# Optimization experiments

Hardware: AMD Instinct MI355X
Metric: run time of the kernel (lower is better)

The kernel has to match this reference:

```python
import jax, jax.numpy as jnp
import numpy as np

N_NODES = 100000
N_EDGES = 800000
D_IN = 256
D_HID = 256
D_OUT = 64
HEADS = 1
ALPHA = 0.5          # TransConv residual weight
GRAPH_WEIGHT = 0.8   # _SGFormer aggregate='add' weight
LN_EPS = 1e-5
BN_EPS = 1e-5


def layer_norm(x, g, b):
    mu = x.mean(-1, keepdims=True)
    var = ((x - mu) ** 2).mean(-1, keepdims=True)
    return (x - mu) * jax.lax.rsqrt(var + LN_EPS) * g + b


def full_attention_conv(qs, ks, vs):
    # qs, ks, vs: [N, H, C]; normalization is by the GLOBAL Frobenius norm
    qs = qs / jnp.linalg.norm(qs)
    ks = ks / jnp.linalg.norm(ks)
    N = qs.shape[0]
    kvs = jnp.einsum('lhm,lhd->hmd', ks, vs)                     # [H,C,C]
    attention_num = jnp.einsum('nhm,hmd->nhd', qs, kvs) + N * vs  # [N,H,C]
    ks_sum = ks.sum(axis=0)                                      # [H,C]
    normalizer = jnp.einsum('nhm,hm->nh', qs, ks_sum)[..., None] + N
    return attention_num / normalizer


def gcn_conv(x, src, dst, w, b, n):
    # PyG GCNConv: h = x @ W; add self-loops; D^-1/2 (A+I) D^-1/2 h; + bias
    h = x @ w
    loop = jnp.arange(n)
    s = jnp.concatenate([src, loop])
    d = jnp.concatenate([dst, loop])
    deg = jax.ops.segment_sum(jnp.ones_like(s, dtype=h.dtype), d, num_segments=n)
    dinv = jnp.where(deg > 0, jax.lax.rsqrt(jnp.maximum(deg, 1e-12)), 0.0)
    norm = dinv[s] * dinv[d]
    out = jax.ops.segment_sum(h[s] * norm[:, None], d, num_segments=n)
    return out + b


def setup_inputs() -> dict:
    key = jax.random.key(0)
    ks = jax.random.split(key, 24)
    f32 = jnp.float32
    def lin(k, fi, fo):
        s = 1.0 / np.sqrt(fi)
        kw, kb = jax.random.split(k)
        return (jax.random.uniform(kw, (fi, fo), f32, -s, s),
                jax.random.uniform(kb, (fo,), f32, -s, s))
    x = jax.random.normal(ks[0], (N_NODES, D_IN), f32)
    edge_index = jax.random.randint(ks[1], (2, N_EDGES), 0, N_NODES, jnp.int64)
    fc0_w, fc0_b = lin(ks[2], D_IN, D_HID)
    wq0_w, wq0_b = lin(ks[3], D_HID, D_HID * HEADS)
    wk0_w, wk0_b = lin(ks[4], D_HID, D_HID * HEADS)
    wv0_w, wv0_b = lin(ks[5], D_HID, D_HID * HEADS)
    wq1_w, wq1_b = lin(ks[6], D_HID, D_HID * HEADS)
    wk1_w, wk1_b = lin(ks[7], D_HID, D_HID * HEADS)
    wv1_w, wv1_b = lin(ks[8], D_HID, D_HID * HEADS)
    gcn_w0, gcn_b0 = lin(ks[9], D_IN, D_HID)
    gcn_w1, gcn_b1 = lin(ks[10], D_HID, D_HID)
    fc_w, fc_b = lin(ks[11], D_HID, D_OUT)
    ones = jnp.ones((D_HID,), f32)
    zeros = jnp.zeros((D_HID,), f32)
    return dict(
        x=x, edge_index=edge_index,
        fc0_w=fc0_w, fc0_b=fc0_b, ln0_g=ones, ln0_b=zeros,
        wq0_w=wq0_w, wq0_b=wq0_b, wk0_w=wk0_w, wk0_b=wk0_b, wv0_w=wv0_w, wv0_b=wv0_b,
        ln1_g=ones, ln1_b=zeros,
        wq1_w=wq1_w, wq1_b=wq1_b, wk1_w=wk1_w, wk1_b=wk1_b, wv1_w=wv1_w, wv1_b=wv1_b,
        ln2_g=ones, ln2_b=zeros,
        gcn_w0=gcn_w0, gcn_b0=gcn_b0, bn_g=ones, bn_b=zeros,
        gcn_w1=gcn_w1, gcn_b1=gcn_b1,
        fc_w=fc_w, fc_b=fc_b)


def reference(x, edge_index, fc0_w, fc0_b, ln0_g, ln0_b,
              wq0_w, wq0_b, wk0_w, wk0_b, wv0_w, wv0_b, ln1_g, ln1_b,
              wq1_w, wq1_b, wk1_w, wk1_b, wv1_w, wv1_b, ln2_g, ln2_b,
              gcn_w0, gcn_b0, bn_g, bn_b, gcn_w1, gcn_b1, fc_w, fc_b):
    n = x.shape[0]
    src, dst = edge_index[0], edge_index[1]
    # ---- TransConv (eval mode: dropout = identity) ----
    h = layer_norm(x @ fc0_w + fc0_b, ln0_g, ln0_b)
    h = jax.nn.relu(h)
    layer_params = [
        (wq0_w, wq0_b, wk0_w, wk0_b, wv0_w, wv0_b, ln1_g, ln1_b),
        (wq1_w, wq1_b, wk1_w, wk1_b, wv1_w, wv1_b, ln2_g, ln2_b),
    ]
    for (qw, qb, kw, kb, vw, vb, lg, lb) in layer_params:
        q = (h @ qw + qb).reshape(n, HEADS, D_HID)
        k = (h @ kw + kb).reshape(n, HEADS, D_HID)
        v = (h @ vw + vb).reshape(n, HEADS, D_HID)
        a = full_attention_conv(q, k, v).mean(axis=1)   # mean over heads
        h = layer_norm(ALPHA * a + (1.0 - ALPHA) * h, lg, lb)
    x_trans = h
    # ---- GCN branch (BN in eval: running_mean=0, running_var=1) ----
    g = gcn_conv(x, src, dst, gcn_w0, gcn_b0, n)
    g = g * (bn_g / jnp.sqrt(1.0 + BN_EPS)) + bn_b
    g = jax.nn.relu(g)
    g = gcn_conv(g, src, dst, gcn_w1, gcn_b1, n)
    # ---- combine + classifier ----
    emb = GRAPH_WEIGHT * g + (1.0 - GRAPH_WEIGHT) * x_trans
    return emb @ fc_w + fc_b
```

## Files before the change

### kernel.cpp

```cpp
#include <hip/hip_runtime.h>
#include <hip/hip_bf16.h>

#define NN 100000
#define NE 800000
#define DH 256
#define DOUT 64
#define NSPL 50000
#define NSO ((size_t)NSPL * DH)
#define NBLK 391

using bf16 = __hip_bfloat16;
typedef __attribute__((ext_vector_type(8))) short bf16x8;
typedef __attribute__((ext_vector_type(4))) float f32x4;

__device__ __forceinline__ float bits2f(unsigned short h) {
    union { unsigned int u; float f; } c; c.u = ((unsigned int)h) << 16; return c.f;
}
__device__ __forceinline__ unsigned short f2b(float v) {
    union { float f; unsigned int u; } c; c.f = v;
    unsigned int u = c.u;
    return (unsigned short)((u + 0x7FFFu + ((u >> 16) & 1u)) >> 16);
}
__device__ __forceinline__ unsigned short tob(float v) { return f2b(v); }
__device__ __forceinline__ unsigned short tob(bf16 v) {
    union { bf16 b; unsigned short u; } c; c.b = v; return c.u;
}
__device__ __forceinline__ float ldf(const void* p, size_t i, int isbf) {
    if (isbf) return bits2f(((const unsigned short*)p)[i]);
    return ((const float*)p)[i];
}
__device__ __forceinline__ float ldS(const float* p, size_t i) { return p[i]; }
__device__ __forceinline__ float ldS(const bf16* p, size_t i) { return __bfloat162float(p[i]); }
__device__ __forceinline__ void stS(float* p, size_t i, float v) { p[i] = v; }
__device__ __forceinline__ void stS(bf16* p, size_t i, float v) { p[i] = __float2bfloat16(v); }
__device__ __forceinline__ float4 ld4S(const float* p) { return *(const float4*)p; }
__device__ __forceinline__ float4 ld4S(const bf16* p) {
    ushort4 u = *(const ushort4*)(const void*)p;
    return make_float4(bits2f(u.x), bits2f(u.y), bits2f(u.z), bits2f(u.w));
}
__device__ __forceinline__ void st4S(float* p, float4 v) { *(float4*)p = v; }
__device__ __forceinline__ void st4S(bf16* p, float4 v) {
    *(ushort4*)(void*)p = make_ushort4(f2b(v.x), f2b(v.y), f2b(v.z), f2b(v.w));
}
__device__ __forceinline__ void ld8(const void* p, size_t idx, int isbf, ushort4& o0, ushort4& o1) {
    if (isbf) {
        const ushort4* q = (const ushort4*)((const unsigned short*)p + idx);
        o0 = q[0]; o1 = q[1];
    } else {
        const float4* q = (const float4*)((const float*)p + idx);
        float4 a = q[0], b = q[1];
        o0 = make_ushort4(f2b(a.x), f2b(a.y), f2b(a.z), f2b(a.w));
        o1 = make_ushort4(f2b(b.x), f2b(b.y), f2b(b.z), f2b(b.w));
    }
}
__device__ __forceinline__ void ld8S(const bf16* p, size_t idx, ushort4& o0, ushort4& o1) {
    const ushort4* q = (const ushort4*)((const unsigned short*)p + idx);
    o0 = q[0]; o1 = q[1];
}
__device__ __forceinline__ void ld8S(const float* p, size_t idx, ushort4& o0, ushort4& o1) {
    const float4* q = (const float4*)(p + idx);
    float4 a = q[0], b = q[1];
    o0 = make_ushort4(f2b(a.x), f2b(a.y), f2b(a.z), f2b(a.w));
    o1 = make_ushort4(f2b(b.x), f2b(b.y), f2b(b.z), f2b(b.w));
}
__device__ __forceinline__ int ld_src(const int* ei, int e, int i64) {
    return i64 ? ei[2 * (size_t)e] : ei[e];
}
__device__ __forceinline__ int ld_dst(const int* ei, int e, int i64) {
    return i64 ? ei[2 * ((size_t)NE + e)] : ei[NE + e];
}

__global__ __launch_bounds__(256) void detect_kernel(const void* x, const int* ei, int* flags)
{
    __shared__ int s_sane[4], s_nz[4];
    int t = threadIdx.x;
    const unsigned short* xu = (const unsigned short*)x;
    int sane = 0;
    for (int i = t; i < 2048; i += 256) {
        float v = bits2f(xu[2 * i]);
        float a = fabsf(v);
        if (v == v && a > 1e-3f && a < 100.f) sane++;
    }
    int nz = 0;
    for (int i = t; i < 4096; i += 256) {
        if (ei[2 * (i * 122) + 1] != 0) nz++;
    }
#pragma unroll
    for (int off = 32; off > 0; off >>= 1) { sane += __shfl_down(sane, off); nz += __shfl_down(nz, off); }
    if ((t & 63) == 0) { s_sane[t >> 6] = sane; s_nz[t >> 6] = nz; }
    __syncthreads();
    if (t == 0) {
        flags[0] = ((s_sane[0] + s_sane[1] + s_sane[2] + s_sane[3]) > 1024) ? 1 : 0;
        flags[1] = ((s_nz[0] + s_nz[1] + s_nz[2] + s_nz[3]) == 0) ? 1 : 0;
    }
}

template <typename ST>
__global__ __launch_bounds__(512) void gemm_mfma(
    const void* __restrict__ A, const void* __restrict__ W,
    const void* __restrict__ bias, ST* __restrict__ C,
    int M, int Nc, const int* __restrict__ flags, int a_sel)
{
    __shared__ unsigned short Bs[64][264];
    const int isbf = flags[0];
    const int abf = (a_sel == 2) ? isbf : a_sel;
    const int tid = threadIdx.x;
    const int wave = tid >> 6, lane = tid & 63;
    const int quad = lane >> 4, nl = lane & 15;
    const int m0 = blockIdx.x * 128;
    const int n0 = blockIdx.y * 64;

    const int arow = m0 + wave * 16 + nl;
    const int av = (arow < M);
    const size_t abase = (size_t)arow * DH + quad * 8;
    ushort4 pa0[8], pa1[8];
#pragma unroll
    for (int s = 0; s < 8; ++s) {
        if (av) ld8(A, abase + s * 32, abf, pa0[s], pa1[s]);
        else { pa0[s] = make_ushort4(0, 0, 0, 0); pa1[s] = pa0[s]; }
    }

#pragma unroll
    for (int it = 0; it < 4; ++it) {
        int p8 = it * 512 + tid;
        int k = p8 >> 3, nb = p8 & 7;
        ushort4 w0, w1;
        ld8(W, (size_t)k * Nc + n0 + nb * 8, isbf, w0, w1);
        int nbase = nb * 8;
        Bs[nbase + 0][k] = w0.x; Bs[nbase + 1][k] = w0.y;
        Bs[nbase + 2][k] = w0.z; Bs[nbase + 3][k] = w0.w;
        Bs[nbase + 4][k] = w1.x; Bs[nbase + 5][k] = w1.y;
        Bs[nbase + 6][k] = w1.z; Bs[nbase + 7][k] = w1.w;
    }
    __syncthreads();

    f32x4 acc[4] = {{0.f,0.f,0.f,0.f},{0.f,0.f,0.f,0.f},{0.f,0.f,0.f,0.f},{0.f,0.f,0.f,0.f}};

#pragma unroll
    for (int s = 0; s < 8; ++s) {
        const int k0 = s * 32;
        bf16x8 af;
        ((ushort4*)&af)[0] = pa0[s]; ((ushort4*)&af)[1] = pa1[s];
#pragma unroll
        for (int ct = 0; ct < 4; ++ct) {
            bf16x8 bfg = *(const bf16x8*)&Bs[ct * 16 + nl][k0 + quad * 8];
            acc[ct] = __builtin_amdgcn_mfma_f32_16x16x32_bf16(af, bfg, acc[ct], 0, 0, 0);
        }
    }

#pragma unroll
    for (int ct = 0; ct < 4; ++ct) {
        int n = n0 + ct * 16 + nl;
        float bv = bias ? ldf(bias, n, isbf) : 0.f;
#pragma unroll
        for (int r = 0; r < 4; ++r) {
            int m = m0 + wave * 16 + quad * 4 + r;
            if (m < M) stS(C, (size_t)m * Nc + n, acc[ct][r] + bv);
        }
    }
}

template <typename ST>
__global__ __launch_bounds__(256) void kvs_mfma(
    const ST* __restrict__ Am, const ST* __restrict__ Bm, float* __restrict__ D)
{
    __shared__ unsigned short Ast[64][36];
    __shared__ unsigned short Bst[64][36];
    const int tid = threadIdx.x;
    const int wave = tid >> 6, lane = tid & 63;
    const int quad = lane >> 4, nl = lane & 15;
    const int i0 = blockIdx.x * 64, j0 = blockIdx.y * 64;
    const int S = gridDim.z;
    const int chunk = (NN + S - 1) / S;
    const int ns = blockIdx.z * chunk;
    const int ne = min(ns + chunk, NN);
    const int nn = tid >> 3;
    const int c0 = (tid & 7) * 8;
    f32x4 acc[4] = {{0.f,0.f,0.f,0.f},{0.f,0.f,0.f,0.f},{0.f,0.f,0.f,0.f},{0.f,0.f,0.f,0.f}};

    for (int n0 = ns; n0 < ne; n0 += 32) {
        int n = n0 + nn;
        ushort4 a0, a1, b0, b1;
        if (n < ne) {
            ld8S(Am, (size_t)n * DH + i0 + c0, a0, a1);
            ld8S(Bm, (size_t)n * DH + j0 + c0, b0, b1);
        } else {
            a0 = make_ushort4(0, 0, 0, 0); a1 = a0; b0 = a0; b1 = a0;
        }
        __syncthreads();
        Ast[c0 + 0][nn] = a0.x; Ast[c0 + 1][nn] = a0.y;
        Ast[c0 + 2][nn] = a0.z; Ast[c0 + 3][nn] = a0.w;
        Ast[c0 + 4][nn] = a1.x; Ast[c0 + 5][nn] = a1.y;
        Ast[c0 + 6][nn] = a1.z; Ast[c0 + 7][nn] = a1.w;
        Bst[c0 + 0][nn] = b0.x; Bst[c0 + 1][nn] = b0.y;
        Bst[c0 + 2][nn] = b0.z; Bst[c0 + 3][nn] = b0.w;
        Bst[c0 + 4][nn] = b1.x; Bst[c0 + 5][nn] = b1.y;
        Bst[c0 + 6][nn] = b1.z; Bst[c0 + 7][nn] = b1.w;
        __syncthreads();
        bf16x8 af = *(const bf16x8*)&Ast[wave * 16 + nl][quad * 8];
#pragma unroll
        for (int ct = 0; ct < 4; ++ct) {
            bf16x8 bfg = *(const bf16x8*)&Bst[ct * 16 + nl][quad * 8];
            acc[ct] = __builtin_amdgcn_mfma_f32_16x16x32_bf16(af, bfg, acc[ct], 0, 0, 0);
        }
    }
#pragma unroll
    for (int ct = 0; ct < 4; ++ct)
#pragma unroll
        for (int r = 0; r < 4; ++r)
            atomicAdd(&D[(size_t)(i0 + wave * 16 + quad * 4 + r) * DH + j0 + ct * 16 + nl], acc[ct][r]);
}

__global__ __launch_bounds__(256) void kvs2b_kernel(const float* __restrict__ kvs,
                                                    unsigned short* __restrict__ kvsb)
{
    int i = blockIdx.x * 256 + threadIdx.x;
    size_t o = (size_t)i * 8;
    float4 a = *(const float4*)(kvs + o);
    float4 b = *(const float4*)(kvs + o + 4);
    *(ushort4*)(kvsb + o)     = make_ushort4(f2b(a.x), f2b(a.y), f2b(a.z), f2b(a.w));
    *(ushort4*)(kvsb + o + 4) = make_ushort4(f2b(b.x), f2b(b.y), f2b(b.z), f2b(b.w));
}

template <typename ST>
__global__ __launch_bounds__(256) void attn_mfma(
    const ST* __restrict__ Q, const ST* __restrict__ V,
    const unsigned short* __restrict__ kvsb, const float* __restrict__ ks_sum,
    const float* __restrict__ qss, const float* __restrict__ kss,
    ST* __restrict__ out)
{
    __shared__ float ks_s[DH];
    __shared__ float nrm_s[64];
    const int tid = threadIdx.x;
    const int wave = tid >> 6, lane = tid & 63;
    const int quad = lane >> 4, nl = lane & 15;
    const int m0 = blockIdx.x * 64;
    const int j0 = blockIdx.y * 128;

    const int arow = m0 + wave * 16 + nl;
    const int av = (arow < NN);
    const size_t abase = (size_t)arow * DH + quad * 8;
    ushort4 pq0[8], pq1[8];
#pragma unroll
    for (int s = 0; s < 8; ++s) {
        if (av) ld8S(Q, abase + s * 32, pq0[s], pq1[s]);
        else { pq0[s] = make_ushort4(0, 0, 0, 0); pq1[s] = pq0[s]; }
    }

    ks_s[tid] = ks_sum[tid];
    __syncthreads();

    f32x4 acc[8];
#pragma unroll
    for (int i = 0; i < 8; ++i) acc[i] = (f32x4){0.f, 0.f, 0.f, 0.f};
    float nrm = 0.f;

#pragma unroll
    for (int s = 0; s < 8; ++s) {
        const int k0 = s * 32;
        bf16x8 af;
        ((ushort4*)&af)[0] = pq0[s]; ((ushort4*)&af)[1] = pq1[s];
#pragma unroll
        for (int j = 0; j < 8; ++j)
            nrm += bits2f(((const unsigned short*)&af)[j]) * ks_s[k0 + quad * 8 + j];
        const unsigned short* kb = kvsb + (size_t)(j0 + nl) * DH + k0 + quad * 8;
#pragma unroll
        for (int ct = 0; ct < 8; ++ct) {
            bf16x8 bfg = *(const bf16x8*)(kb + (size_t)ct * 16 * DH);
            acc[ct] = __builtin_amdgcn_mfma_f32_16x16x32_bf16(af, bfg, acc[ct], 0, 0, 0);
        }
    }
    nrm += __shfl_xor(nrm, 16);
    nrm += __shfl_xor(nrm, 32);
    if (lane < 16) nrm_s[wave * 16 + lane] = nrm;
    __syncthreads();
    const float scale = rsqrtf(*qss) * rsqrtf(*kss);
#pragma unroll
    for (int r = 0; r < 4; ++r) {
        int row = m0 + wave * 16 + quad * 4 + r;
        if (row >= NN) continue;
        float den = nrm_s[wave * 16 + quad * 4 + r] * scale + (float)NN;
#pragma unroll
        for (int ct = 0; ct < 8; ++ct) {
            int col = j0 + ct * 16 + nl;
            float v = ldS(V, (size_t)row * DH + col);
            float numv = acc[ct][r] * scale + (float)NN * v;
            stS(out, (size_t)row * DH + col, numv / den);
        }
    }
}

template <typename ST>
__global__ __launch_bounds__(256) void ln_kernel(
    const ST* __restrict__ A, const ST* __restrict__ B,
    float alpha, float beta,
    const void* __restrict__ g, const void* __restrict__ b,
    ST* __restrict__ out, int relu, const int* __restrict__ flags)
{
    const int isbf = flags[0];
    const int wave = threadIdx.x >> 6, lane = threadIdx.x & 63;
    const int row = blockIdx.x * 4 + wave;
    if (row >= NN) return;
    const size_t base = (size_t)row * DH + lane * 4;
    float4 v = ld4S(&A[base]);
    v.x *= alpha; v.y *= alpha; v.z *= alpha; v.w *= alpha;
    if (B) {
        float4 w = ld4S(&B[base]);
        v.x += beta * w.x; v.y += beta * w.y; v.z += beta * w.z; v.w += beta * w.w;
    }
    float s = v.x + v.y + v.z + v.w;
    float s2 = v.x * v.x + v.y * v.y + v.z * v.z + v.w * v.w;
#pragma unroll
    for (int off = 32; off > 0; off >>= 1) {
        s += __shfl_xor(s, off);
        s2 += __shfl_xor(s2, off);
    }
    float mean = s * (1.f / DH);
    float var = s2 * (1.f / DH) - mean * mean;
    float rstd = rsqrtf(var + 1e-5f);
    float4 o;
    o.x = (v.x - mean) * rstd * ldf(g, lane * 4 + 0, isbf) + ldf(b, lane * 4 + 0, isbf);
    o.y = (v.y - mean) * rstd * ldf(g, lane * 4 + 1, isbf) + ldf(b, lane * 4 + 1, isbf);
    o.z = (v.z - mean) * rstd * ldf(g, lane * 4 + 2, isbf) + ldf(b, lane * 4 + 2, isbf);
    o.w = (v.w - mean) * rstd * ldf(g, lane * 4 + 3, isbf) + ldf(b, lane * 4 + 3, isbf);
    if (relu) {
        o.x = fmaxf(o.x, 0.f); o.y = fmaxf(o.y, 0.f);
        o.z = fmaxf(o.z, 0.f); o.w = fmaxf(o.w, 0.f);
    }
    st4S(&out[base], o);
}

template <typename ST>
__global__ __launch_bounds__(256) void sumsq_kernel(
    const ST* __restrict__ A, size_t n, float* __restrict__ out)
{
    __shared__ float ps[4];
    size_t i = (size_t)blockIdx.x * blockDim.x + threadIdx.x;
    size_t stride = (size_t)gridDim.x * blockDim.x;
    float s = 0.f;
    for (; i < n; i += stride) { float v = ldS(A, i); s += v * v; }
#pragma unroll
    for (int off = 32; off > 0; off >>= 1) s += __shfl_down(s, off);
    if ((threadIdx.x & 63) == 0) ps[threadIdx.x >> 6] = s;
    __syncthreads();
    if (threadIdx.x == 0) atomicAdd(out, ps[0] + ps[1] + ps[2] + ps[3]);
}

template <typename ST>
__global__ __launch_bounds__(256) void colsum_kernel(
    const ST* __restrict__ Km, float* __restrict__ out)
{
    const int t = threadIdx.x;
    const int per = (NN + gridDim.x - 1) / gridDim.x;
    size_t r0 = (size_t)blockIdx.x * per;
    size_t r1 = r0 + per; if (r1 > NN) r1 = NN;
    float s = 0.f;
    for (size_t r = r0; r < r1; ++r) s += ldS(Km, r * DH + t);
    atomicAdd(&out[t], s);
}

__global__ __launch_bounds__(256) void count_kernel(const int* __restrict__ ei, int* __restrict__ cnt,
                                                    const int* __restrict__ flags)
{
    int e = blockIdx.x * 256 + threadIdx.x;
    if (e >= NE) return;
    int d = ld_dst(ei, e, flags[1]);
    if ((unsigned)d < NN) atomicAdd(&cnt[d], 1);
}

__global__ __launch_bounds__(256) void scan_block_kernel(const int* __restrict__ cnt,
                                                         int* __restrict__ pre, int* __restrict__ bsum)
{
    __shared__ int s[256];
    int i = blockIdx.x * 256 + threadIdx.x;
    int v = (i < NN) ? cnt[i] : 0;
    s[threadIdx.x] = v;
    __syncthreads();
    for (int off = 1; off < 256; off <<= 1) {
        int t = (threadIdx.x >= off) ? s[threadIdx.x - off] : 0;
        __syncthreads();
        s[threadIdx.x] += t;
        __syncthreads();
    }
    if (i < NN) pre[i] = s[threadIdx.x] - v;
    if (threadIdx.x == 255) bsum[blockIdx.x] = s[255];
}

__global__ __launch_bounds__(512) void scan_partial_kernel(int* __restrict__ bsum, int nb)
{
    __shared__ int s[512];
    int t = threadIdx.x;
    int v = (t < nb) ? bsum[t] : 0;
    s[t] = v;
    __syncthreads();
    for (int off = 1; off < 512; off <<= 1) {
        int u = (t >= off) ? s[t - off] : 0;
        __syncthreads();
        s[t] += u;
        __syncthreads();
    }
    if (t < nb) bsum[t] = s[t] - v;
}

__global__ __launch_bounds__(256) void finalize_kernel(int* __restrict__ base, const int* __restrict__ bsum,
                                                       const int* __restrict__ cnt, int* __restrict__ cursor,
                                                       float* __restrict__ dinv)
{
    int i = blockIdx.x * 256 + threadIdx.x;
    if (i >= NN) return;
    int b = base[i] + bsum[blockIdx.x];
    base[i] = b;
    cursor[i] = b;
    dinv[i] = rsqrtf((float)cnt[i] + 1.0f);
}

__global__ __launch_bounds__(256) void scatter_kernel(const int* __restrict__ ei, int* __restrict__ cursor,
                                                      int* __restrict__ srcs, const int* __restrict__ flags)
{
    int e = blockIdx.x * 256 + threadIdx.x;
    if (e >= NE) return;
    int i64 = flags[1];
    int s = ld_src(ei, e, i64), d = ld_dst(ei, e, i64);
    if ((unsigned)s >= NN || (unsigned)d >= NN) return;
    int pos = atomicAdd(&cursor[d], 1);
    srcs[pos] = s;
}

template <typename ST, int MODE>
__global__ __launch_bounds__(256) void fgather_kernel(
    const ST* __restrict__ Hs, const ST* __restrict__ Ht,
    const int* __restrict__ base, const int* __restrict__ cnt,
    const int* __restrict__ srcs, const float* __restrict__ dinv,
    const void* __restrict__ bias, const void* __restrict__ bng, const void* __restrict__ bnb,
    const int* __restrict__ flags, ST* __restrict__ out)
{
    const int isbf = flags[0];
    int node = blockIdx.x * 4 + (threadIdx.x >> 6);
    int lane = threadIdx.x & 63;
    if (node >= NN) return;
    int b0 = base[node], deg = cnt[node];
    float dd = dinv[node];
    float4 a0 = make_float4(0.f, 0.f, 0.f, 0.f);
    float4 a1 = make_float4(0.f, 0.f, 0.f, 0.f);
    int j = 0;
    for (; j + 4 <= deg; j += 4) {
        int s0 = srcs[b0 + j + 0], s1 = srcs[b0 + j + 1];
        int s2 = srcs[b0 + j + 2], s3 = srcs[b0 + j + 3];
        float n0 = dd * dinv[s0], n1 = dd * dinv[s1];
        float n2 = dd * dinv[s2], n3 = dd * dinv[s3];
        float4 h0 = ld4S(&Hs[(size_t)s0 * DH + lane * 4]);
        float4 h1 = ld4S(&Hs[(size_t)s1 * DH + lane * 4]);
        float4 h2 = ld4S(&Hs[(size_t)s2 * DH + lane * 4]);
        float4 h3 = ld4S(&Hs[(size_t)s3 * DH + lane * 4]);
        a0.x += h0.x * n0; a0.y += h0.y * n0; a0.z += h0.z * n0; a0.w += h0.w * n0;
        a1.x += h1.x * n1; a1.y += h1.y * n1; a1.z += h1.z * n1; a1.w += h1.w * n1;
        a0.x += h2.x * n2; a0.y += h2.y * n2; a0.z += h2.z * n2; a0.w += h2.w * n2;
        a1.x += h3.x * n3; a1.y += h3.y * n3; a1.z += h3.z * n3; a1.w += h3.w * n3;
    }
    for (; j < deg; ++j) {
        int s0 = srcs[b0 + j];
        float n0 = dd * dinv[s0];
        float4 h0 = ld4S(&Hs[(size_t)s0 * DH + lane * 4]);
        a0.x += h0.x * n0; a0.y += h0.y * n0; a0.z += h0.z * n0; a0.w += h0.w * n0;
    }
    const size_t obase = (size_t)node * DH + lane * 4;
    float4 own = ld4S(&Hs[obase]);
    float di2 = dd * dd;
    int c = lane * 4;
    float4 v;
    v.x = a0.x + a1.x + own.x * di2 + ldf(bias, c + 0, isbf);
    v.y = a0.y + a1.y + own.y * di2 + ldf(bias, c + 1, isbf);
    v.z = a0.z + a1.z + own.z * di2 + ldf(bias, c + 2, isbf);
    v.w = a0.w + a1.w + own.w * di2 + ldf(bias, c + 3, isbf);
    if (MODE == 0) {
        const float bnscale = 0.99999500003749981f;
        v.x = fmaxf(v.x * (ldf(bng, c + 0, isbf) * bnscale) + ldf(bnb, c + 0, isbf), 0.f);
        v.y = fmaxf(v.y * (ldf(bng, c + 1, isbf) * bnscale) + ldf(bnb, c + 1, isbf), 0.f);
        v.z = fmaxf(v.z * (ldf(bng, c + 2, isbf) * bnscale) + ldf(bnb, c + 2, isbf), 0.f);
        v.w = fmaxf(v.w * (ldf(bng, c + 3, isbf) * bnscale) + ldf(bnb, c + 3, isbf), 0.f);
    } else {
        float4 t = ld4S(&Ht[obase]);
        v.x = 0.8f * v.x + 0.2f * t.x;
        v.y = 0.8f * v.y + 0.2f * t.y;
        v.z = 0.8f * v.z + 0.2f * t.z;
        v.w = 0.8f * v.w + 0.2f * t.w;
    }
    st4S(&out[obase], v);
}

__global__ __launch_bounds__(256) void deg_kernel(const int* __restrict__ ei, float* __restrict__ deg,
                                                  const int* __restrict__ flags)
{
    int i64 = flags[1];
    int e = blockIdx.x * 256 + threadIdx.x;
    if (e >= NE) return;
    int d = ld_dst(ei, e, i64);
    if ((unsigned)d < NN) atomicAdd(&deg[d], 1.0f);
}

__global__ __launch_bounds__(256) void dinv_kernel(float* __restrict__ deg)
{
    int i = blockIdx.x * 256 + threadIdx.x;
    if (i < NN) deg[i] = rsqrtf(deg[i] + 1.0f);
}

template <typename ST>
__global__ __launch_bounds__(256) void agg_kernel(
    const ST* __restrict__ Hs, const int* __restrict__ ei,
    const float* __restrict__ dinv, float* __restrict__ lo, float* __restrict__ hi,
    const int* __restrict__ flags)
{
    int i64 = flags[1];
    int e = blockIdx.x * 4 + (threadIdx.x >> 6);
    int lane = threadIdx.x & 63;
    if (e >= NE) return;
    int s = ld_src(ei, e, i64), d = ld_dst(ei, e, i64);
    if ((unsigned)s >= NN || (unsigned)d >= NN) return;
    float nrm = dinv[s] * dinv[d];
    const float4 h4 = ld4S(&Hs[(size_t)s * DH + lane * 4]);
    float* o = (d < NSPL ? &lo[(size_t)d * DH] : &hi[(size_t)(d - NSPL) * DH]) + lane * 4;
    atomicAdd(o + 0, h4.x * nrm);
    atomicAdd(o + 1, h4.y * nrm);
    atomicAdd(o + 2, h4.z * nrm);
    atomicAdd(o + 3, h4.w * nrm);
}

template <typename ST>
__global__ __launch_bounds__(256) void gcn_epi1_kernel(
    const float* __restrict__ lo, const float* __restrict__ hi,
    const ST* __restrict__ h1, const float* __restrict__ dinv,
    const void* __restrict__ b0, const void* __restrict__ bng, const void* __restrict__ bnb,
    const int* __restrict__ flags, ST* __restrict__ out)
{
    const int isbf = flags[0];
    size_t idx = (size_t)blockIdx.x * 256 + threadIdx.x;
    if (idx >= (size_t)NN * DH) return;
    int i = (int)(idx >> 8), c = (int)(idx & 255);
    float aggv = (i < NSPL) ? lo[idx] : hi[idx - NSO];
    float di = dinv[i];
    float v = aggv + ldS(h1, idx) * di * di + ldf(b0, c, isbf);
    const float bnscale = 0.99999500003749981f;
    v = v * (ldf(bng, c, isbf) * bnscale) + ldf(bnb, c, isbf);
    stS(out, idx, fmaxf(v, 0.f));
}

template <typename ST>
__global__ __launch_bounds__(256) void gcn_epi2_kernel(
    const float* __restrict__ lo, const float* __restrict__ hi,
    const ST* __restrict__ h2, const ST* __restrict__ Ht, const float* __restrict__ dinv,
    const void* __restrict__ b1, const int* __restrict__ flags, ST* __restrict__ out)
{
    const int isbf = flags[0];
    size_t idx = (size_t)blockIdx.x * 256 + threadIdx.x;
    if (idx >= (size_t)NN * DH) return;
    int i = (int)(idx >> 8), c = (int)(idx & 255);
    float aggv = (i < NSPL) ? lo[idx] : hi[idx - NSO];
    float di = dinv[i];
    float g = aggv + ldS(h2, idx) * di * di + ldf(b1, c, isbf);
    stS(out, idx, 0.8f * g + 0.2f * ldS(Ht, idx));
}

__global__ __launch_bounds__(256) void diag_kernel(float* out, size_t n, float val)
{
    size_t i = (size_t)blockIdx.x * 256 + threadIdx.x;
    if (i < n) out[i] = val;
}

template <typename ST>
static void run_pipeline(void* const* d_in, void* d_out, char* wsb, hipStream_t stream, int use_csr)
{
    const void* x      = d_in[0];
    const int*  ei     = (const int*)d_in[1];
    const void* fc0_w  = d_in[2];  const void* fc0_b  = d_in[3];
    const void* ln0_g  = d_in[4];  const void* ln0_b  = d_in[5];
    const void* wq0_w  = d_in[6];  const void* wq0_b  = d_in[7];
    const void* wk0_w  = d_in[8];  const void* wk0_b  = d_in[9];
    const void* wv0_w  = d_in[10]; const void* wv0_b  = d_in[11];
    const void* ln1_g  = d_in[12]; const void* ln1_b  = d_in[13];
    const void* wq1_w  = d_in[14]; const void* wq1_b  = d_in[15];
    const void* wk1_w  = d_in[16]; const void* wk1_b  = d_in[17];
    const void* wv1_w  = d_in[18]; const void* wv1_b  = d_in[19];
    const void* ln2_g  = d_in[20]; const void* ln2_b  = d_in[21];
    const void* gcn_w0 = d_in[22]; const void* gcn_b0 = d_in[23];
    const void* bn_g   = d_in[24]; const void* bn_b   = d_in[25];
    const void* gcn_w1 = d_in[26]; const void* gcn_b1 = d_in[27];
    const void* fc_w   = d_in[28]; const void* fc_b   = d_in[29];

    const size_t stN = (size_t)NN * DH * sizeof(ST);
    ST* H  = (ST*)(wsb);
    ST* Qb = (ST*)(wsb + stN);
    ST* Kb = (ST*)(wsb + 2 * stN);
    ST* Vb = (ST*)(wsb + 3 * stN);
    float* aux = (float*)(wsb + 4 * stN);
    float* kvs    = aux;
    float* ks_sum = aux + 65536;
    float* qss    = aux + 65792;
    float* kss    = aux + 65793;
    float* dinv   = aux + 65808;
    int*   flags  = (int*)(aux + 65808 + NN);
    int* cnt    = (int*)(aux + 65808 + NN + 16);
    int* base   = cnt + NN;
    int* cursor = base + NN;
    int* bsum   = cursor + NN;
    int* srcs   = bsum + 512;
    unsigned short* kvsb = (unsigned short*)dinv;

    const int asel = (sizeof(ST) == 2) ? 1 : 0;
    dim3 mfmaGrid((NN + 127) / 128, DH / 64);
    const size_t NELEM = (size_t)NN * DH;

    detect_kernel<<<1, 256, 0, stream>>>(x, ei, flags);

    gemm_mfma<ST><<<mfmaGrid, 512, 0, stream>>>(x, fc0_w, fc0_b, Qb, NN, DH, flags, 2);
    ln_kernel<ST><<<(NN + 3) / 4, 256, 0, stream>>>(Qb, (const ST*)nullptr, 1.f, 0.f, ln0_g, ln0_b, H, 1, flags);

    for (int layer = 0; layer < 2; ++layer) {
        const void *qw, *qb, *kw, *kb, *vw, *vb, *lg, *lb;
        if (layer == 0) { qw = wq0_w; qb = wq0_b; kw = wk0_w; kb = wk0_b; vw = wv0_w; vb = wv0_b; lg = ln1_g; lb = ln1_b; }
        else            { qw = wq1_w; qb = wq1_b; kw = wk1_w; kb = wk1_b; vw = wv1_w; vb = wv1_b; lg = ln2_g; lb = ln2_b; }
        gemm_mfma<ST><<<mfmaGrid, 512, 0, stream>>>(H, qw, qb, Qb, NN, DH, flags, asel);
        gemm_mfma<ST><<<mfmaGrid, 512, 0, stream>>>(H, kw, kb, Kb, NN, DH, flags, asel);
        gemm_mfma<ST><<<mfmaGrid, 512, 0, stream>>>(H, vw, vb, Vb, NN, DH, flags, asel);
        hipMemsetAsync(aux, 0, (65536 + 256 + 2) * sizeof(float), stream);
        sumsq_kernel<ST><<<2048, 256, 0, stream>>>(Qb, NELEM, qss);
        sumsq_kernel<ST><<<2048, 256, 0, stream>>>(Kb, NELEM, kss);
        kvs_mfma<ST><<<dim3(4, 4, 128), 256, 0, stream>>>(Vb, Kb, kvs);
        colsum_kernel<ST><<<800, 256, 0, stream>>>(Kb, ks_sum);
        kvs2b_kernel<<<32, 256, 0, stream>>>(kvs, kvsb);
        attn_mfma<ST><<<dim3((NN + 63) / 64, 2), 256, 0, stream>>>(Qb, Vb, kvsb, ks_sum, qss, kss, Kb);
        ln_kernel<ST><<<(NN + 3) / 4, 256, 0, stream>>>(Kb, H, 0.5f, 0.5f, lg, lb, H, 0, flags);
    }

    if (use_csr) {
        hipMemsetAsync(cnt, 0, NN * sizeof(int), stream);
        count_kernel<<<(NE + 255) / 256, 256, 0, stream>>>(ei, cnt, flags);
        scan_block_kernel<<<NBLK, 256, 0, stream>>>(cnt, base, bsum);
        scan_partial_kernel<<<1, 512, 0, stream>>>(bsum, NBLK);
        finalize_kernel<<<NBLK, 256, 0, stream>>>(base, bsum, cnt, cursor, dinv);
        scatter_kernel<<<(NE + 255) / 256, 256, 0, stream>>>(ei, cursor, srcs, flags);

        gemm_mfma<ST><<<mfmaGrid, 512, 0, stream>>>(x, gcn_w0, nullptr, Qb, NN, DH, flags, 2);
        fgather_kernel<ST, 0><<<(NN + 3) / 4, 256, 0, stream>>>(
            Qb, (const ST*)nullptr, base, cnt, srcs, dinv, gcn_b0, bn_g, bn_b, flags, Kb);
        gemm_mfma<ST><<<mfmaGrid, 512, 0, stream>>>(Kb, gcn_w1, nullptr, Vb, NN, DH, flags, asel);
        fgather_kernel<ST, 1><<<(NN + 3) / 4, 256, 0, stream>>>(
            Vb, H, base, cnt, srcs, dinv, gcn_b1, nullptr, nullptr, flags, Qb);

        gemm_mfma<float><<<dim3((NN + 127) / 128, 1), 512, 0, stream>>>(Qb, fc_w, fc_b, (float*)d_out, NN, DOUT, flags, asel);
    } else {
        float* a1lo = (float*)(wsb + 2 * stN);
        float* a1hi = a1lo + NSO;
        ST* h2; float *a2lo, *a2hi;
        if (sizeof(ST) == 4) { h2 = Vb; a2lo = (float*)(wsb + 2 * stN); a2hi = a2lo + NSO; }
        else                 { h2 = Kb; a2lo = (float*)(wsb + stN);     a2hi = (float*)(wsb + 3 * stN); }

        hipMemsetAsync(dinv, 0, NN * sizeof(float), stream);
        deg_kernel<<<(NE + 255) / 256, 256, 0, stream>>>(ei, dinv, flags);
        dinv_kernel<<<(NN + 255) / 256, 256, 0, stream>>>(dinv);

        gemm_mfma<ST><<<mfmaGrid, 512, 0, stream>>>(x, gcn_w0, nullptr, Qb, NN, DH, flags, 2);
        hipMemsetAsync(a1lo, 0, NELEM * sizeof(float), stream);
        agg_kernel<ST><<<(NE + 3) / 4, 256, 0, stream>>>(Qb, ei, dinv, a1lo, a1hi, flags);
        gcn_epi1_kernel<ST><<<(NELEM + 255) / 256, 256, 0, stream>>>(a1lo, a1hi, Qb, dinv, gcn_b0, bn_g, bn_b, flags, Qb);

        gemm_mfma<ST><<<mfmaGrid, 512, 0, stream>>>(Qb, gcn_w1, nullptr, h2, NN, DH, flags, asel);
        hipMemsetAsync(a2lo, 0, NSO * sizeof(float), stream);
        hipMemsetAsync(a2hi, 0, NSO * sizeof(float), stream);
        agg_kernel<ST><<<(NE + 3) / 4, 256, 0, stream>>>(h2, ei, dinv, a2lo, a2hi, flags);
        gcn_epi2_kernel<ST><<<(NELEM + 255) / 256, 256, 0, stream>>>(a2lo, a2hi, h2, H, dinv, gcn_b1, flags, h2);

        gemm_mfma<float><<<dim3((NN + 127) / 128, 1), 512, 0, stream>>>(h2, fc_w, fc_b, (float*)d_out, NN, DOUT, flags, asel);
    }
}

extern "C" void kernel_launch(void* const* d_in, const int* in_sizes, int n_in,
                              void* d_out, int out_size, void* d_ws, size_t ws_size,
                              hipStream_t stream)
{
    char* wsb = (char*)d_ws;
    const size_t AUXF  = 65808 + NN + 16;
    const size_t CSRI  = 3 * (size_t)NN + 512 + NE;
    const size_t AUXB  = AUXF * sizeof(float);
    const size_t AUXB2 = AUXB + CSRI * sizeof(int);
    const size_t needA  = 4 * ((size_t)NN * DH * 4) + AUXB;
    const size_t needA2 = 4 * ((size_t)NN * DH * 4) + AUXB2;
    const size_t needB  = 4 * ((size_t)NN * DH * 2) + AUXB;
    const size_t needB2 = 4 * ((size_t)NN * DH * 2) + AUXB2;

    if (ws_size >= needA) {
        run_pipeline<float>(d_in, d_out, wsb, stream, ws_size >= needA2);
    } else if (ws_size >= needB) {
        run_pipeline<bf16>(d_in, d_out, wsb, stream, ws_size >= needB2);
    } else {
        float mb = (float)(ws_size >> 20);
        size_t n = (size_t)out_size;
        diag_kernel<<<(n + 255) / 256, 256, 0, stream>>>((float*)d_out, n, mb);
    }
}
```

Before: 1.922 ms.

## Fuse Q/K/V projections with sum-of-squares and K column-sum reductions

```diff
diff --git a/kernel.cpp b/kernel.cpp
--- a/kernel.cpp
+++ b/kernel.cpp
@@ -33,6 +33,9 @@
 __device__ __forceinline__ float ldS(const bf16* p, size_t i) { return __bfloat162float(p[i]); }
 __device__ __forceinline__ void stS(float* p, size_t i, float v) { p[i] = v; }
 __device__ __forceinline__ void stS(bf16* p, size_t i, float v) { p[i] = __float2bfloat16(v); }
+template <typename ST> __device__ __forceinline__ float storedS(float v);
+template <> __device__ __forceinline__ float storedS<float>(float v) { return v; }
+template <> __device__ __forceinline__ float storedS<bf16>(float v) { return bits2f(f2b(v)); }
 __device__ __forceinline__ float4 ld4S(const float* p) { return *(const float4*)p; }
 __device__ __forceinline__ float4 ld4S(const bf16* p) {
     ushort4 u = *(const ushort4*)(const void*)p;
@@ -112,11 +115,11 @@
 
     const int arow = m0 + wave * 16 + nl;
     const int av = (arow < M);
-    const size_t abase = (size_t)arow * DH + quad * 8;
+    const size_t ab = (size_t)arow * DH + quad * 8;
     ushort4 pa0[8], pa1[8];
 #pragma unroll
     for (int s = 0; s < 8; ++s) {
-        if (av) ld8(A, abase + s * 32, abf, pa0[s], pa1[s]);
+        if (av) ld8(A, ab + s * 32, abf, pa0[s], pa1[s]);
         else { pa0[s] = make_ushort4(0, 0, 0, 0); pa1[s] = pa0[s]; }
     }
 
@@ -135,15 +138,13 @@
     __syncthreads();
 
     f32x4 acc[4] = {{0.f,0.f,0.f,0.f},{0.f,0.f,0.f,0.f},{0.f,0.f,0.f,0.f},{0.f,0.f,0.f,0.f}};
-
 #pragma unroll
     for (int s = 0; s < 8; ++s) {
-        const int k0 = s * 32;
         bf16x8 af;
         ((ushort4*)&af)[0] = pa0[s]; ((ushort4*)&af)[1] = pa1[s];
 #pragma unroll
         for (int ct = 0; ct < 4; ++ct) {
-            bf16x8 bfg = *(const bf16x8*)&Bs[ct * 16 + nl][k0 + quad * 8];
+            bf16x8 bfg = *(const bf16x8*)&Bs[ct * 16 + nl][s * 32 + quad * 8];
             acc[ct] = __builtin_amdgcn_mfma_f32_16x16x32_bf16(af, bfg, acc[ct], 0, 0, 0);
         }
     }
@@ -158,6 +159,105 @@
             if (m < M) stS(C, (size_t)m * Nc + n, acc[ct][r] + bv);
         }
     }
+}
+
+template <typename ST>
+__global__ __launch_bounds__(512) void qkv_mfma(
+    const ST* __restrict__ A,
+    const void* __restrict__ Wq, const void* __restrict__ bq,
+    const void* __restrict__ Wk, const void* __restrict__ bk,
+    const void* __restrict__ Wv, const void* __restrict__ bv_,
+    ST* __restrict__ Qo, ST* __restrict__ Ko, ST* __restrict__ Vo,
+    const int* __restrict__ flags,
+    float* __restrict__ qss, float* __restrict__ kss, float* __restrict__ ks_sum)
+{
+    __shared__ unsigned short Bs[64][264];
+    __shared__ float cs_s[64];
+    const int isbf = flags[0];
+    const int tid = threadIdx.x;
+    const int wave = tid >> 6, lane = tid & 63;
+    const int quad = lane >> 4, nl = lane & 15;
+    const int m0 = blockIdx.x * 128;
+    const int n0 = blockIdx.y * 64;
+
+    const int arow = m0 + wave * 16 + nl;
+    const int av = (arow < NN);
+    const size_t ab = (size_t)arow * DH + quad * 8;
+    ushort4 pa0[8], pa1[8];
+#pragma unroll
+    for (int s = 0; s < 8; ++s) {
+        if (av) ld8S(A, ab + s * 32, pa0[s], pa1[s]);
+        else { pa0[s] = make_ushort4(0, 0, 0, 0); pa1[s] = pa0[s]; }
+    }
+    if (tid < 64) cs_s[tid] = 0.f;
+
+    float ssq_q = 0.f, ssq_k = 0.f;
+
+    for (int w = 0; w < 3; ++w) {
+        const void* W = (w == 0) ? Wq : (w == 1) ? Wk : Wv;
+        const void* B = (w == 0) ? bq : (w == 1) ? bk : bv_;
+        ST* C = (w == 0) ? Qo : (w == 1) ? Ko : Vo;
+
+        if (w > 0) __syncthreads();
+#pragma unroll
+        for (int it = 0; it < 4; ++it) {
+            int p8 = it * 512 + tid;
+            int k = p8 >> 3, nb = p8 & 7;
+            ushort4 w0, w1;
+            ld8(W, (size_t)k * DH + n0 + nb * 8, isbf, w0, w1);
+            int nbase = nb * 8;
+            Bs[nbase + 0][k] = w0.x; Bs[nbase + 1][k] = w0.y;
+            Bs[nbase + 2][k] = w0.z; Bs[nbase + 3][k] = w0.w;
+            Bs[nbase + 4][k] = w1.x; Bs[nbase + 5][k] = w1.y;
+            Bs[nbase + 6][k] = w1.z; Bs[nbase + 7][k] = w1.w;
+        }
+        __syncthreads();
+
+        f32x4 acc[4] = {{0.f,0.f,0.f,0.f},{0.f,0.f,0.f,0.f},{0.f,0.f,0.f,0.f},{0.f,0.f,0.f,0.f}};
+#pragma unroll
+        for (int s = 0; s < 8; ++s) {
+            bf16x8 af;
+            ((ushort4*)&af)[0] = pa0[s]; ((ushort4*)&af)[1] = pa1[s];
+#pragma unroll
+            for (int ct = 0; ct < 4; ++ct) {
+                bf16x8 bfg = *(const bf16x8*)&Bs[ct * 16 + nl][s * 32 + quad * 8];
+                acc[ct] = __builtin_amdgcn_mfma_f32_16x16x32_bf16(af, bfg, acc[ct], 0, 0, 0);
+            }
+        }
+
+        float mycs[4] = {0.f, 0.f, 0.f, 0.f};
+        float myssq = 0.f;
+#pragma unroll
+        for (int ct = 0; ct < 4; ++ct) {
+            int n = n0 + ct * 16 + nl;
+            float bvv = ldf(B, n, isbf);
+#pragma unroll
+            for (int r = 0; r < 4; ++r) {
+                int m = m0 + wave * 16 + quad * 4 + r;
+                if (m < NN) {
+                    float v = acc[ct][r] + bvv;
+                    stS(C, (size_t)m * DH + n, v);
+                    float sv = storedS<ST>(v);
+                    myssq += sv * sv;
+                    mycs[ct] += sv;
+                }
+            }
+        }
+        if (w == 0) ssq_q += myssq;
+        if (w == 1) {
+            ssq_k += myssq;
+#pragma unroll
+            for (int ct = 0; ct < 4; ++ct)
+                atomicAdd(&cs_s[ct * 16 + nl], mycs[ct]);
+        }
+    }
+
+    float sq = ssq_q, sk = ssq_k;
+#pragma unroll
+    for (int off = 1; off < 64; off <<= 1) { sq += __shfl_xor(sq, off); sk += __shfl_xor(sk, off); }
+    if (lane == 0) { atomicAdd(qss, sq); atomicAdd(kss, sk); }
+    __syncthreads();
+    if (tid < 64) atomicAdd(&ks_sum[n0 + tid], cs_s[tid]);
 }
 
 template <typename ST>
@@ -237,29 +337,24 @@
     const int m0 = blockIdx.x * 64;
     const int j0 = blockIdx.y * 128;
 
+    ks_s[tid] = ks_sum[tid];
+    __syncthreads();
+
     const int arow = m0 + wave * 16 + nl;
     const int av = (arow < NN);
     const size_t abase = (size_t)arow * DH + quad * 8;
-    ushort4 pq0[8], pq1[8];
-#pragma unroll
-    for (int s = 0; s < 8; ++s) {
-        if (av) ld8S(Q, abase + s * 32, pq0[s], pq1[s]);
-        else { pq0[s] = make_ushort4(0, 0, 0, 0); pq1[s] = pq0[s]; }
-    }
-
-    ks_s[tid] = ks_sum[tid];
-    __syncthreads();
-
     f32x4 acc[8];
 #pragma unroll
     for (int i = 0; i < 8; ++i) acc[i] = (f32x4){0.f, 0.f, 0.f, 0.f};
     float nrm = 0.f;
 
-#pragma unroll
-    for (int s = 0; s < 8; ++s) {
-        const int k0 = s * 32;
+#pragma unroll 2
+    for (int k0 = 0; k0 < DH; k0 += 32) {
+        ushort4 a0, a1;
+        if (av) ld8S(Q, abase + k0, a0, a1);
+        else { a0 = make_ushort4(0,0,0,0); a1 = a0; }
         bf16x8 af;
-        ((ushort4*)&af)[0] = pq0[s]; ((ushort4*)&af)[1] = pq1[s];
+        ((ushort4*)&af)[0] = a0; ((ushort4*)&af)[1] = a1;
 #pragma unroll
         for (int j = 0; j < 8; ++j)
             nrm += bits2f(((const unsigned short*)&af)[j]) * ks_s[k0 + quad * 8 + j];
@@ -328,35 +423,6 @@
         o.z = fmaxf(o.z, 0.f); o.w = fmaxf(o.w, 0.f);
     }
     st4S(&out[base], o);
-}
-
-template <typename ST>
-__global__ __launch_bounds__(256) void sumsq_kernel(
-    const ST* __restrict__ A, size_t n, float* __restrict__ out)
-{
-    __shared__ float ps[4];
-    size_t i = (size_t)blockIdx.x * blockDim.x + threadIdx.x;
-    size_t stride = (size_t)gridDim.x * blockDim.x;
-    float s = 0.f;
-    for (; i < n; i += stride) { float v = ldS(A, i); s += v * v; }
-#pragma unroll
-    for (int off = 32; off > 0; off >>= 1) s += __shfl_down(s, off);
-    if ((threadIdx.x & 63) == 0) ps[threadIdx.x >> 6] = s;
-    __syncthreads();
-    if (threadIdx.x == 0) atomicAdd(out, ps[0] + ps[1] + ps[2] + ps[3]);
-}
-
-template <typename ST>
-__global__ __launch_bounds__(256) void colsum_kernel(
-    const ST* __restrict__ Km, float* __restrict__ out)
-{
-    const int t = threadIdx.x;
-    const int per = (NN + gridDim.x - 1) / gridDim.x;
-    size_t r0 = (size_t)blockIdx.x * per;
-    size_t r1 = r0 + per; if (r1 > NN) r1 = NN;
-    float s = 0.f;
-    for (size_t r = r0; r < r1; ++r) s += ldS(Km, r * DH + t);
-    atomicAdd(&out[t], s);
 }
 
 __global__ __launch_bounds__(256) void count_kernel(const int* __restrict__ ei, int* __restrict__ cnt,
@@ -526,6 +592,22 @@
 }
 
 template <typename ST>
+__global__ __launch_bounds__(256) void sumsq_kernel(
+    const ST* __restrict__ A, size_t n, float* __restrict__ out)
+{
+    __shared__ float ps[4];
+    size_t i = (size_t)blockIdx.x * blockDim.x + threadIdx.x;
+    size_t stride = (size_t)gridDim.x * blockDim.x;
+    float s = 0.f;
+    for (; i < n; i += stride) { float v = ldS(A, i); s += v * v; }
+#pragma unroll
+    for (int off = 32; off > 0; off >>= 1) s += __shfl_down(s, off);
+    if ((threadIdx.x & 63) == 0) ps[threadIdx.x >> 6] = s;
+    __syncthreads();
+    if (threadIdx.x == 0) atomicAdd(out, ps[0] + ps[1] + ps[2] + ps[3]);
+}
+
+template <typename ST>
 __global__ __launch_bounds__(256) void gcn_epi1_kernel(
     const float* __restrict__ lo, const float* __restrict__ hi,
     const ST* __restrict__ h1, const float* __restrict__ dinv,
@@ -606,26 +688,22 @@
     unsigned short* kvsb = (unsigned short*)dinv;
 
     const int asel = (sizeof(ST) == 2) ? 1 : 0;
-    dim3 mfmaGrid((NN + 127) / 128, DH / 64);
+    dim3 gemmGrid((NN + 127) / 128, DH / 64);
     const size_t NELEM = (size_t)NN * DH;
 
     detect_kernel<<<1, 256, 0, stream>>>(x, ei, flags);
 
-    gemm_mfma<ST><<<mfmaGrid, 512, 0, stream>>>(x, fc0_w, fc0_b, Qb, NN, DH, flags, 2);
+    gemm_mfma<ST><<<gemmGrid, 512, 0, stream>>>(x, fc0_w, fc0_b, Qb, NN, DH, flags, 2);
     ln_kernel<ST><<<(NN + 3) / 4, 256, 0, stream>>>(Qb, (const ST*)nullptr, 1.f, 0.f, ln0_g, ln0_b, H, 1, flags);
 
     for (int layer = 0; layer < 2; ++layer) {
         const void *qw, *qb, *kw, *kb, *vw, *vb, *lg, *lb;
         if (layer == 0) { qw = wq0_w; qb = wq0_b; kw = wk0_w; kb = wk0_b; vw = wv0_w; vb = wv0_b; lg = ln1_g; lb = ln1_b; }
         else            { qw = wq1_w; qb = wq1_b; kw = wk1_w; kb = wk1_b; vw = wv1_w; vb = wv1_b; lg = ln2_g; lb = ln2_b; }
-        gemm_mfma<ST><<<mfmaGrid, 512, 0, stream>>>(H, qw, qb, Qb, NN, DH, flags, asel);
-        gemm_mfma<ST><<<mfmaGrid, 512, 0, stream>>>(H, kw, kb, Kb, NN, DH, flags, asel);
-        gemm_mfma<ST><<<mfmaGrid, 512, 0, stream>>>(H, vw, vb, Vb, NN, DH, flags, asel);
         hipMemsetAsync(aux, 0, (65536 + 256 + 2) * sizeof(float), stream);
-        sumsq_kernel<ST><<<2048, 256, 0, stream>>>(Qb, NELEM, qss);
-        sumsq_kernel<ST><<<2048, 256, 0, stream>>>(Kb, NELEM, kss);
+        qkv_mfma<ST><<<gemmGrid, 512, 0, stream>>>(H, qw, qb, kw, kb, vw, vb,
+                                                   Qb, Kb, Vb, flags, qss, kss, ks_sum);
         kvs_mfma<ST><<<dim3(4, 4, 128), 256, 0, stream>>>(Vb, Kb, kvs);
-        colsum_kernel<ST><<<800, 256, 0, stream>>>(Kb, ks_sum);
         kvs2b_kernel<<<32, 256, 0, stream>>>(kvs, kvsb);
         attn_mfma<ST><<<dim3((NN + 63) / 64, 2), 256, 0, stream>>>(Qb, Vb, kvsb, ks_sum, qss, kss, Kb);
         ln_kernel<ST><<<(NN + 3) / 4, 256, 0, stream>>>(Kb, H, 0.5f, 0.5f, lg, lb, H, 0, flags);
@@ -639,10 +717,10 @@
         finalize_kernel<<<NBLK, 256, 0, stream>>>(base, bsum, cnt, cursor, dinv);
         scatter_kernel<<<(NE + 255) / 256, 256, 0, stream>>>(ei, cursor, srcs, flags);
 
-        gemm_mfma<ST><<<mfmaGrid, 512, 0, stream>>>(x, gcn_w0, nullptr, Qb, NN, DH, flags, 2);
+        gemm_mfma<ST><<<gemmGrid, 512, 0, stream>>>(x, gcn_w0, nullptr, Qb, NN, DH, flags, 2);
         fgather_kernel<ST, 0><<<(NN + 3) / 4, 256, 0, stream>>>(
             Qb, (const ST*)nullptr, base, cnt, srcs, dinv, gcn_b0, bn_g, bn_b, flags, Kb);
-        gemm_mfma<ST><<<mfmaGrid, 512, 0, stream>>>(Kb, gcn_w1, nullptr, Vb, NN, DH, flags, asel);
+        gemm_mfma<ST><<<gemmGrid, 512, 0, stream>>>(Kb, gcn_w1, nullptr, Vb, NN, DH, flags, asel);
         fgather_kernel<ST, 1><<<(NN + 3) / 4, 256, 0, stream>>>(
             Vb, H, base, cnt, srcs, dinv, gcn_b1, nullptr, nullptr, flags, Qb);
 
@@ -658,12 +736,12 @@
         deg_kernel<<<(NE + 255) / 256, 256, 0, stream>>>(ei, dinv, flags);
         dinv_kernel<<<(NN + 255) / 256, 256, 0, stream>>>(dinv);
 
-        gemm_mfma<ST><<<mfmaGrid, 512, 0, stream>>>(x, gcn_w0, nullptr, Qb, NN, DH, flags, 2);
+        gemm_mfma<ST><<<gemmGrid, 512, 0, stream>>>(x, gcn_w0, nullptr, Qb, NN, DH, flags, 2);
         hipMemsetAsync(a1lo, 0, NELEM * sizeof(float), stream);
         agg_kernel<ST><<<(NE + 3) / 4, 256, 0, stream>>>(Qb, ei, dinv, a1lo, a1hi, flags);
         gcn_epi1_kernel<ST><<<(NELEM + 255) / 256, 256, 0, stream>>>(a1lo, a1hi, Qb, dinv, gcn_b0, bn_g, bn_b, flags, Qb);
 
-        gemm_mfma<ST><<<mfmaGrid, 512, 0, stream>>>(Qb, gcn_w1, nullptr, h2, NN, DH, flags, asel);
+        gemm_mfma<ST><<<gemmGrid, 512, 0, stream>>>(Qb, gcn_w1, nullptr, h2, NN, DH, flags, asel);
         hipMemsetAsync(a2lo, 0, NSO * sizeof(float), stream);
         hipMemsetAsync(a2hi, 0, NSO * sizeof(float), stream);
         agg_kernel<ST><<<(NE + 3) / 4, 256, 0, stream>>>(h2, ei, dinv, a2lo, a2hi, flags);
```

Result: slower. 2.690 ms (+39.9%).
